# Optimization experiments

Hardware: AMD Instinct MI355X
Metric: run time of the kernel (lower is better)

The kernel has to match this reference:

```python
import jax, jax.numpy as jnp
import numpy as np

N_NODES = 100000
N_EDGES = 1600000
IN_DIM, HID_DIM, N_CLASSES = 128, 64, 40


def spmm(edge_row, edge_col, edge_val, dense):
    # sparse [N,N] @ dense [N,D] via gather + segment-sum over edges
    msgs = edge_val[:, None] * dense[edge_col]            # [E, D]
    return jax.ops.segment_sum(msgs, edge_row, num_segments=N_NODES)


def setup_inputs() -> dict:
    key = jax.random.key(0)
    ks = jax.random.split(key, 8)
    x = jax.random.normal(ks[0], (N_NODES, IN_DIM), dtype=jnp.float32)
    edge_row = jax.random.randint(ks[1], (N_EDGES,), 0, N_NODES, dtype=jnp.int32)
    edge_col = jax.random.randint(ks[2], (N_EDGES,), 0, N_NODES, dtype=jnp.int32)
    edge_val = jax.random.uniform(ks[3], (N_EDGES,), dtype=jnp.float32)
    s1 = 1.0 / np.sqrt(IN_DIM)
    s2 = 1.0 / np.sqrt(HID_DIM)
    W1 = jax.random.normal(ks[4], (IN_DIM, HID_DIM), dtype=jnp.float32) * s1
    b1 = jnp.zeros((HID_DIM,), dtype=jnp.float32)
    W2 = jax.random.normal(ks[5], (HID_DIM, HID_DIM), dtype=jnp.float32) * s2
    b2 = jnp.zeros((HID_DIM,), dtype=jnp.float32)
    Wc = jax.random.normal(ks[6], (HID_DIM, N_CLASSES), dtype=jnp.float32) * s2
    bc = jnp.zeros((N_CLASSES,), dtype=jnp.float32)
    return {"x": x, "edge_row": edge_row, "edge_col": edge_col, "edge_val": edge_val,
            "W1": W1, "b1": b1, "W2": W2, "b2": b2, "Wc": Wc, "bc": bc}


def reference(x, edge_row, edge_col, edge_val, W1, b1, W2, b2, Wc, bc):
    # GCN layer 1: support = xW+b, aggregate, relu  (dropout off in eval)
    h = jax.nn.relu(spmm(edge_row, edge_col, edge_val, x @ W1 + b1))
    # GCN layer 2
    h = spmm(edge_row, edge_col, edge_val, h @ W2 + b2)
    # node classifier + log-softmax
    logits = h @ Wc + bc
    return jax.nn.log_softmax(logits, axis=-1)
```

## Files before the change

kernel.cpp:

```cpp
#include <hip/hip_runtime.h>

#define N_NODES   100000
#define N_EDGES   1600000
#define IN_DIM    128
#define HID_DIM   64
#define N_CLASSES 40
#define U_DIM     40

#define NBUCK 782
#define BCAP  2816
#define EPB   6400
#define PBLK  1024
#define GRID_A 250

typedef __attribute__((ext_vector_type(8))) short bf16x8;
typedef __attribute__((ext_vector_type(4))) float f32x4;

__device__ inline short f2bf(float f) {
    unsigned u = __float_as_uint(f);
    unsigned r = (u + 0x7FFFu + ((u >> 16) & 1u)) >> 16;
    return (short)r;
}
__device__ inline float bflo(unsigned w) { return __uint_as_float(w << 16); }
__device__ inline float bfhi(unsigned w) { return __uint_as_float(w & 0xFFFF0000u); }
__device__ inline float upval(unsigned w) { return __uint_as_float((w >> 17) << 16); }

__global__ __launch_bounds__(PBLK) void prep_parta(const int* __restrict__ erow,
                                                   const int* __restrict__ ecol,
                                                   const float* __restrict__ eval,
                                                   int* __restrict__ bcnt,
                                                   int2* __restrict__ tmp,
                                                   const float* __restrict__ W1,
                                                   const float* __restrict__ W2,
                                                   const float* __restrict__ Wc,
                                                   const float* __restrict__ b2,
                                                   short* __restrict__ W1t,
                                                   short* __restrict__ Mt,
                                                   float* __restrict__ bv) {
    __shared__ int2 pay[EPB];
    __shared__ int hist[NBUCK], lbase[NBUCK], cur[NBUCK], dofs[NBUCK], scan[NBUCK];
    int tid = threadIdx.x;
    if (blockIdx.x >= GRID_A) {
        int pb = blockIdx.x - GRID_A;
        {
            int i = pb * PBLK + tid;
            if (i < IN_DIM * HID_DIM) {
                int n = i >> 7, k = i & 127;
                W1t[i] = f2bf(W1[k * HID_DIM + n]);
            }
        }
        if (pb == 0) {
            for (int idx = tid; idx < HID_DIM * HID_DIM; idx += PBLK) {
                int n = idx >> 6, i = idx & 63;
                float acc = 0.f;
                if (n < N_CLASSES)
                    for (int j = 0; j < HID_DIM; ++j)
                        acc = fmaf(W2[i * HID_DIM + j], Wc[j * N_CLASSES + n], acc);
                Mt[n * HID_DIM + i] = f2bf(acc);
            }
        }
        if (pb == 1 && tid < N_CLASSES) {
            float acc = 0.f;
            for (int j = 0; j < HID_DIM; ++j)
                acc = fmaf(b2[j], Wc[j * N_CLASSES + tid], acc);
            bv[tid] = acc;
        }
        return;
    }
    int e0 = blockIdx.x * EPB;
    for (int i = tid; i < NBUCK; i += PBLK) { hist[i] = 0; cur[i] = 0; }
    __syncthreads();
    for (int i = tid; i < EPB; i += PBLK)
        atomicAdd(&hist[erow[e0 + i] >> 7], 1);
    __syncthreads();
    for (int i = tid; i < NBUCK; i += PBLK) {
        int n = hist[i];
        dofs[i] = i * BCAP + (n ? atomicAdd(&bcnt[i], n) : 0);
        scan[i] = n;
    }
    __syncthreads();
    for (int off = 1; off < NBUCK; off <<= 1) {
        int t = 0;
        if (tid < NBUCK && tid >= off) t = scan[tid - off];
        __syncthreads();
        if (tid < NBUCK) scan[tid] += t;
        __syncthreads();
    }
    if (tid < NBUCK) {
        lbase[tid] = scan[tid] - hist[tid];
        dofs[tid] -= lbase[tid];
    }
    __syncthreads();
    for (int i = tid; i < EPB; i += PBLK) {
        int e = e0 + i;
        int r = erow[e];
        int b = r >> 7;
        int p = lbase[b] + atomicAdd(&cur[b], 1);
        unsigned u = __float_as_uint(eval[e]);
        unsigned vb = ((u + 0x7FFFu + ((u >> 16) & 1u)) >> 16) & 0x7FFFu;
        pay[p] = make_int2(((r & 127) << 17) | ecol[e], (int)((vb << 10) | (unsigned)b));
    }
    __syncthreads();
    for (int p = tid; p < EPB; p += PBLK) {
        int2 v = pay[p];
        int b = (unsigned)v.y & 1023u;
        int dest = dofs[b] + p;
        if (dest < (b + 1) * BCAP)
            tmp[dest] = v;
    }
}

__global__ __launch_bounds__(256) void part_b_gemm1(const int* __restrict__ bcnt,
                                                    const int2* __restrict__ tmp,
                                                    unsigned* __restrict__ tmp2,
                                                    int2* __restrict__ rowmeta,
                                                    const float* __restrict__ x,
                                                    const short* __restrict__ W1t,
                                                    const float* __restrict__ b1,
                                                    unsigned short* __restrict__ outH) {
    __shared__ int2 ein[BCAP];
    __shared__ unsigned eout[BCAP];
    __shared__ int hist[128], pad[128], basep[128], cur[128], scan[128];
    if (blockIdx.x < NBUCK) {
        int b = blockIdx.x;
        int nb = bcnt[b]; if (nb > BCAP) nb = BCAP;
        for (int i = threadIdx.x; i < nb; i += 256) ein[i] = tmp[(size_t)b * BCAP + i];
        if (threadIdx.x < 128) { hist[threadIdx.x] = 0; cur[threadIdx.x] = 0; }
        __syncthreads();
        for (int i = threadIdx.x; i < nb; i += 256)
            atomicAdd(&hist[(ein[i].x >> 17) & 127], 1);
        __syncthreads();
        if (threadIdx.x < 128) {
            pad[threadIdx.x] = (hist[threadIdx.x] + 3) & ~3;
            scan[threadIdx.x] = pad[threadIdx.x];
        }
        __syncthreads();
        for (int off = 1; off < 128; off <<= 1) {
            int t = 0;
            if (threadIdx.x < 128 && threadIdx.x >= off) t = scan[threadIdx.x - off];
            __syncthreads();
            if (threadIdx.x < 128) scan[threadIdx.x] += t;
            __syncthreads();
        }
        if (threadIdx.x < 128) basep[threadIdx.x] = scan[threadIdx.x] - pad[threadIdx.x];
        __syncthreads();
        int ntot = scan[127]; if (ntot > BCAP) ntot = BCAP;
        for (int i = threadIdx.x; i < nb; i += 256) {
            int lr = (ein[i].x >> 17) & 127;
            int p = basep[lr] + atomicAdd(&cur[lr], 1);
            if (p < BCAP) {
                unsigned vb = ((unsigned)ein[i].y >> 10) & 0x7FFFu;
                eout[p] = (vb << 17) | (unsigned)(ein[i].x & 0x1FFFF);
            }
        }
        __syncthreads();
        if (threadIdx.x < 128) {
            int pe = basep[threadIdx.x] + pad[threadIdx.x];
            for (int p = basep[threadIdx.x] + hist[threadIdx.x]; p < pe && p < BCAP; ++p)
                eout[p] = 0u;
        }
        __syncthreads();
        for (int i = threadIdx.x; i < ntot; i += 256) tmp2[(size_t)b * BCAP + i] = eout[i];
        if (threadIdx.x < 128) {
            int r = b * 128 + threadIdx.x;
            if (r < N_NODES)
                rowmeta[r] = make_int2(b * BCAP + basep[threadIdx.x], pad[threadIdx.x]);
        }
    } else {
        int gb = blockIdx.x - NBUCK;
        int wave = threadIdx.x >> 6;
        int lane = threadIdx.x & 63;
        int node0 = gb * 64 + wave * 16;
        if (node0 >= N_NODES) return;
        int m = lane & 15;
        int q = lane >> 4;
        const float* xrow = x + (size_t)(node0 + m) * IN_DIM;
        f32x4 acc0 = {0,0,0,0}, acc1 = {0,0,0,0}, acc2 = {0,0,0,0}, acc3 = {0,0,0,0};
#pragma unroll
        for (int kb = 0; kb < 4; ++kb) {
            int k0 = kb * 32 + q * 8;
            float4 a0 = *(const float4*)(xrow + k0);
            float4 a1 = *(const float4*)(xrow + k0 + 4);
            bf16x8 af;
            af[0]=f2bf(a0.x); af[1]=f2bf(a0.y); af[2]=f2bf(a0.z); af[3]=f2bf(a0.w);
            af[4]=f2bf(a1.x); af[5]=f2bf(a1.y); af[6]=f2bf(a1.z); af[7]=f2bf(a1.w);
            bf16x8 bf0 = *(const bf16x8*)(W1t + ( 0 + m) * IN_DIM + k0);
            bf16x8 bf1 = *(const bf16x8*)(W1t + (16 + m) * IN_DIM + k0);
            bf16x8 bf2 = *(const bf16x8*)(W1t + (32 + m) * IN_DIM + k0);
            bf16x8 bf3 = *(const bf16x8*)(W1t + (48 + m) * IN_DIM + k0);
            acc0 = __builtin_amdgcn_mfma_f32_16x16x32_bf16(af, bf0, acc0, 0, 0, 0);
            acc1 = __builtin_amdgcn_mfma_f32_16x16x32_bf16(af, bf1, acc1, 0, 0, 0);
            acc2 = __builtin_amdgcn_mfma_f32_16x16x32_bf16(af, bf2, acc2, 0, 0, 0);
            acc3 = __builtin_amdgcn_mfma_f32_16x16x32_bf16(af, bf3, acc3, 0, 0, 0);
        }
        f32x4 accs[4] = {acc0, acc1, acc2, acc3};
#pragma unroll
        for (int t = 0; t < 4; ++t) {
            float bias = b1[t * 16 + m];
#pragma unroll
            for (int r = 0; r < 4; ++r) {
                int node = node0 + q * 4 + r;
                outH[(size_t)node * HID_DIM + t * 16 + m] = (unsigned short)f2bf(accs[t][r] + bias);
            }
        }
    }
}

#define FMA8(v,g) \
    a0=fmaf(v,bflo(g.x),a0); a1=fmaf(v,bfhi(g.x),a1); a2=fmaf(v,bflo(g.y),a2); a3=fmaf(v,bfhi(g.y),a3); \
    a4=fmaf(v,bflo(g.z),a4); a5=fmaf(v,bfhi(g.z),a5); a6=fmaf(v,bflo(g.w),a6); a7=fmaf(v,bfhi(g.w),a7);

__global__ __launch_bounds__(256) void spmm1_mm(const int2* __restrict__ rowmeta,
                                                const unsigned* __restrict__ ecv,
                                                const unsigned short* __restrict__ dense,
                                                const short* __restrict__ Mt,
                                                unsigned short* __restrict__ outU) {
    __shared__ unsigned lm[4][8][68];
    __shared__ unsigned short tr[32][64];
    int wave = threadIdx.x >> 6;
    int lane = threadIdx.x & 63;
    int s = lane >> 3, dq = lane & 7;
    int row = wave * 8 + s;
    int r = blockIdx.x * 32 + row;
    int2 meta = rowmeta[r];
    int beg = meta.x, deg = meta.y;
    int degc = deg < 64 ? deg : 64;
    for (int e = dq * 2; e < degc; e += 16)
        *(uint2*)&lm[wave][s][e] = *(const uint2*)(ecv + beg + e);
    __syncthreads();
    const unsigned* mp = lm[wave][s];
    float a0=0,a1=0,a2=0,a3=0,a4=0,a5=0,a6=0,a7=0;
#define LDG(wv) (*(const uint4*)(dense + ((size_t)((wv) & 0x1FFFF) << 6) + (dq << 3)))
    if (deg > 0) {
        int e = 0;
        if (degc & 4) {
            uint4 w = *(const uint4*)mp;
            uint4 g0 = LDG(w.x), g1 = LDG(w.y), g2 = LDG(w.z), g3 = LDG(w.w);
            float v0 = upval(w.x), v1 = upval(w.y), v2 = upval(w.z), v3 = upval(w.w);
            FMA8(v0,g0); FMA8(v1,g1); FMA8(v2,g2); FMA8(v3,g3);
            e = 4;
        }
        for (; e < degc; e += 8) {
            uint4 wa = *(const uint4*)(mp + e);
            uint4 wb = *(const uint4*)(mp + e + 4);
            uint4 g0 = LDG(wa.x), g1 = LDG(wa.y), g2 = LDG(wa.z), g3 = LDG(wa.w);
            uint4 g4 = LDG(wb.x), g5 = LDG(wb.y), g6 = LDG(wb.z), g7 = LDG(wb.w);
            float v0 = upval(wa.x), v1 = upval(wa.y), v2 = upval(wa.z), v3 = upval(wa.w);
            float v4 = upval(wb.x), v5 = upval(wb.y), v6 = upval(wb.z), v7 = upval(wb.w);
            FMA8(v0,g0); FMA8(v1,g1); FMA8(v2,g2); FMA8(v3,g3);
            FMA8(v4,g4); FMA8(v5,g5); FMA8(v6,g6); FMA8(v7,g7);
        }
        for (int e2 = 64; e2 < deg; ++e2) {
            unsigned we = ecv[beg + e2];
            uint4 g = LDG(we);
            float v = upval(we);
            FMA8(v,g);
        }
    }
#undef LDG
    uint4 o;
    o.x = (unsigned short)f2bf(fmaxf(a0,0.f)) | ((unsigned)(unsigned short)f2bf(fmaxf(a1,0.f)) << 16);
    o.y = (unsigned short)f2bf(fmaxf(a2,0.f)) | ((unsigned)(unsigned short)f2bf(fmaxf(a3,0.f)) << 16);
    o.z = (unsigned short)f2bf(fmaxf(a4,0.f)) | ((unsigned)(unsigned short)f2bf(fmaxf(a5,0.f)) << 16);
    o.w = (unsigned short)f2bf(fmaxf(a6,0.f)) | ((unsigned)(unsigned short)f2bf(fmaxf(a7,0.f)) << 16);
    *(uint4*)(&tr[row][(dq ^ s) << 3]) = o;
    __syncthreads();
    int m = lane & 15;
    int q = lane >> 4;
    int nt = wave >> 1;
    int tb = (wave & 1) << 1;
    int arow = nt * 16 + m;
    f32x4 c0 = {0,0,0,0}, c1 = {0,0,0,0};
#pragma unroll
    for (int kb = 0; kb < 2; ++kb) {
        int ch = kb * 4 + q;
        bf16x8 af = *(const bf16x8*)(&tr[arow][(ch ^ (arow & 7)) << 3]);
        int k0 = kb * 32 + q * 8;
        bf16x8 bf0 = *(const bf16x8*)(Mt + ((tb + 0) * 16 + m) * HID_DIM + k0);
        bf16x8 bf1 = *(const bf16x8*)(Mt + ((tb + 1) * 16 + m) * HID_DIM + k0);
        c0 = __builtin_amdgcn_mfma_f32_16x16x32_bf16(af, bf0, c0, 0, 0, 0);
        c1 = __builtin_amdgcn_mfma_f32_16x16x32_bf16(af, bf1, c1, 0, 0, 0);
    }
#pragma unroll
    for (int rr = 0; rr < 4; ++rr) {
        int node = blockIdx.x * 32 + nt * 16 + q * 4 + rr;
        int col0 = tb * 16 + m;
        int col1 = col0 + 16;
        if (col0 < U_DIM)
            outU[(size_t)node * U_DIM + col0] = (unsigned short)f2bf(c0[rr]);
        if (col1 < U_DIM)
            outU[(size_t)node * U_DIM + col1] = (unsigned short)f2bf(c1[rr]);
    }
}

__global__ __launch_bounds__(256) void spmm_cls(const int2* __restrict__ rowmeta,
                                                const unsigned* __restrict__ ecv,
                                                const unsigned short* __restrict__ dense,
                                                const float* __restrict__ bv,
                                                const float* __restrict__ bc,
                                                float* __restrict__ outF) {
    __shared__ unsigned lm[4][8][68];
    int wave = threadIdx.x >> 6;
    int lane = threadIdx.x & 63;
    int s = lane >> 3, dq = lane & 7;
    int dof = (dq < 5 ? dq : 0) << 3;
    int r = (blockIdx.x * 4 + wave) * 8 + s;
    float4 bv0 = {0,0,0,0}, bv1 = {0,0,0,0}, bc0 = {0,0,0,0}, bc1 = {0,0,0,0};
    if (dq < 5) {
        bv0 = *(const float4*)(bv + dq * 8);  bv1 = *(const float4*)(bv + dq * 8 + 4);
        bc0 = *(const float4*)(bc + dq * 8);  bc1 = *(const float4*)(bc + dq * 8 + 4);
    }
    int2 meta = rowmeta[r];
    int beg = meta.x, deg = meta.y;
    int degc = deg < 64 ? deg : 64;
    for (int e = dq * 2; e < degc; e += 16)
        *(uint2*)&lm[wave][s][e] = *(const uint2*)(ecv + beg + e);
    __syncthreads();
    const unsigned* mp = lm[wave][s];
    float a0=0,a1=0,a2=0,a3=0,a4=0,a5=0,a6=0,a7=0, asum=0;
#define LDU(wv) (*(const uint4*)(dense + (size_t)((wv) & 0x1FFFF) * U_DIM + dof))
    if (deg > 0) {
        int e = 0;
        if (degc & 4) {
            uint4 w = *(const uint4*)mp;
            uint4 g0 = LDU(w.x), g1 = LDU(w.y), g2 = LDU(w.z), g3 = LDU(w.w);
            float v0 = upval(w.x), v1 = upval(w.y), v2 = upval(w.z), v3 = upval(w.w);
            asum += v0 + v1 + v2 + v3;
            FMA8(v0,g0); FMA8(v1,g1); FMA8(v2,g2); FMA8(v3,g3);
            e = 4;
        }
        for (; e < degc; e += 8) {
            uint4 wa = *(const uint4*)(mp + e);
            uint4 wb = *(const uint4*)(mp + e + 4);
            uint4 g0 = LDU(wa.x), g1 = LDU(wa.y), g2 = LDU(wa.z), g3 = LDU(wa.w);
            uint4 g4 = LDU(wb.x), g5 = LDU(wb.y), g6 = LDU(wb.z), g7 = LDU(wb.w);
            float v0 = upval(wa.x), v1 = upval(wa.y), v2 = upval(wa.z), v3 = upval(wa.w);
            float v4 = upval(wb.x), v5 = upval(wb.y), v6 = upval(wb.z), v7 = upval(wb.w);
            asum += v0 + v1 + v2 + v3 + v4 + v5 + v6 + v7;
            FMA8(v0,g0); FMA8(v1,g1); FMA8(v2,g2); FMA8(v3,g3);
            FMA8(v4,g4); FMA8(v5,g5); FMA8(v6,g6); FMA8(v7,g7);
        }
        for (int e2 = 64; e2 < deg; ++e2) {
            unsigned we = ecv[beg + e2];
            uint4 g = LDU(we);
            float v = upval(we);
            asum += v;
            FMA8(v,g);
        }
    }
#undef LDU
    float l0 = fmaf(asum, bv0.x, a0) + bc0.x;
    float l1 = fmaf(asum, bv0.y, a1) + bc0.y;
    float l2 = fmaf(asum, bv0.z, a2) + bc0.z;
    float l3 = fmaf(asum, bv0.w, a3) + bc0.w;
    float l4 = fmaf(asum, bv1.x, a4) + bc1.x;
    float l5 = fmaf(asum, bv1.y, a5) + bc1.y;
    float l6 = fmaf(asum, bv1.z, a6) + bc1.z;
    float l7 = fmaf(asum, bv1.w, a7) + bc1.w;
    float mx = -1e30f;
    if (dq < 5)
        mx = fmaxf(fmaxf(fmaxf(l0, l1), fmaxf(l2, l3)),
                   fmaxf(fmaxf(l4, l5), fmaxf(l6, l7)));
#pragma unroll
    for (int off = 1; off < 8; off <<= 1) mx = fmaxf(mx, __shfl_xor(mx, off));
    float ss = 0.f;
    if (dq < 5)
        ss = __expf(l0 - mx) + __expf(l1 - mx) + __expf(l2 - mx) + __expf(l3 - mx)
           + __expf(l4 - mx) + __expf(l5 - mx) + __expf(l6 - mx) + __expf(l7 - mx);
#pragma unroll
    for (int off = 1; off < 8; off <<= 1) ss += __shfl_xor(ss, off);
    float lse = mx + __logf(ss);
    if (dq < 5) {
        float4 o0 = {l0 - lse, l1 - lse, l2 - lse, l3 - lse};
        float4 o1 = {l4 - lse, l5 - lse, l6 - lse, l7 - lse};
        float* dst = outF + (size_t)r * N_CLASSES + dq * 8;
        *(float4*)(dst) = o0;
        *(float4*)(dst + 4) = o1;
    }
}

extern "C" void kernel_launch(void* const* d_in, const int* in_sizes, int n_in,
                              void* d_out, int out_size, void* d_ws, size_t ws_size,
                              hipStream_t stream) {
    const float* x    = (const float*)d_in[0];
    const int*   erow = (const int*)  d_in[1];
    const int*   ecol = (const int*)  d_in[2];
    const float* eval = (const float*)d_in[3];
    const float* W1   = (const float*)d_in[4];
    const float* b1   = (const float*)d_in[5];
    const float* W2   = (const float*)d_in[6];
    const float* b2   = (const float*)d_in[7];
    const float* Wc   = (const float*)d_in[8];
    const float* bc   = (const float*)d_in[9];
    float* out = (float*)d_out;

    char* ws = (char*)d_ws;
    size_t off = 0;
    auto alloc = [&](size_t bytes) { char* p = ws + off; off += (bytes + 255) & ~(size_t)255; return p; };
    unsigned short* bufA = (unsigned short*)alloc((size_t)N_NODES * HID_DIM * sizeof(short));
    unsigned short* bufB = (unsigned short*)alloc((size_t)N_NODES * U_DIM * sizeof(short));
    int2*     tmp     = (int2*)    alloc((size_t)NBUCK * BCAP * sizeof(int2));
    unsigned* tmp2    = (unsigned*)alloc((size_t)NBUCK * BCAP * sizeof(unsigned));
    int2*     rowmeta = (int2*)    alloc((size_t)N_NODES * sizeof(int2));
    int*      bcnt    = (int*)     alloc(NBUCK * sizeof(int));
    short*    W1t     = (short*)   alloc((size_t)IN_DIM * HID_DIM * sizeof(short));
    short*    Mt      = (short*)   alloc((size_t)HID_DIM * HID_DIM * sizeof(short));
    float*    bv      = (float*)   alloc(64 * sizeof(float));

    const int tile_grid = (N_NODES + 63) / 64;
    const int spmm_grid = N_NODES / 32;

    hipMemsetAsync(bcnt, 0, NBUCK * sizeof(int), stream);
    prep_parta<<<GRID_A + 8, PBLK, 0, stream>>>(erow, ecol, eval, bcnt, tmp,
                                                W1, W2, Wc, b2, W1t, Mt, bv);
    part_b_gemm1<<<NBUCK + tile_grid, 256, 0, stream>>>(bcnt, tmp, tmp2, rowmeta,
                                                        x, W1t, b1, bufA);
    spmm1_mm<<<spmm_grid, 256, 0, stream>>>(rowmeta, tmp2, bufA, Mt, bufB);
    spmm_cls<<<spmm_grid, 256, 0, stream>>>(rowmeta, tmp2, bufB, bv, bc, out);
}
```

Baseline: 218.4 us.

## Use wave-shuffle scans, halve edges per partition block, pad U rows to 64

```diff
diff --git a/kernel.cpp b/kernel.cpp
--- a/kernel.cpp
+++ b/kernel.cpp
@@ -6,12 +6,13 @@
 #define HID_DIM   64
 #define N_CLASSES 40
 #define U_DIM     40
+#define U_STRIDE  64
 
 #define NBUCK 782
 #define BCAP  2816
-#define EPB   6400
+#define EPB   3200
 #define PBLK  1024
-#define GRID_A 250
+#define GRID_A 500
 
 typedef __attribute__((ext_vector_type(8))) short bf16x8;
 typedef __attribute__((ext_vector_type(4))) float f32x4;
@@ -38,7 +39,8 @@
                                                    short* __restrict__ Mt,
                                                    float* __restrict__ bv) {
     __shared__ int2 pay[EPB];
-    __shared__ int hist[NBUCK], lbase[NBUCK], cur[NBUCK], dofs[NBUCK], scan[NBUCK];
+    __shared__ int hist[NBUCK], lbase[NBUCK], cur[NBUCK], dofs[NBUCK];
+    __shared__ int wscan[16];
     int tid = threadIdx.x;
     if (blockIdx.x >= GRID_A) {
         int pb = blockIdx.x - GRID_A;
@@ -76,19 +78,33 @@
     for (int i = tid; i < NBUCK; i += PBLK) {
         int n = hist[i];
         dofs[i] = i * BCAP + (n ? atomicAdd(&bcnt[i], n) : 0);
-        scan[i] = n;
-    }
-    __syncthreads();
-    for (int off = 1; off < NBUCK; off <<= 1) {
-        int t = 0;
-        if (tid < NBUCK && tid >= off) t = scan[tid - off];
-        __syncthreads();
-        if (tid < NBUCK) scan[tid] += t;
-        __syncthreads();
-    }
-    if (tid < NBUCK) {
-        lbase[tid] = scan[tid] - hist[tid];
-        dofs[tid] -= lbase[tid];
+    }
+    __syncthreads();
+    {
+        int lane = tid & 63, wv = tid >> 6;
+        int val = (tid < NBUCK) ? hist[tid] : 0;
+#pragma unroll
+        for (int off = 1; off < 64; off <<= 1) {
+            int t = __shfl_up(val, off);
+            if (lane >= off) val += t;
+        }
+        if (lane == 63) wscan[wv] = val;
+        __syncthreads();
+        if (wv == 0) {
+            int s = (lane < 16) ? wscan[lane] : 0;
+#pragma unroll
+            for (int off = 1; off < 16; off <<= 1) {
+                int t = __shfl_up(s, off);
+                if (lane >= off) s += t;
+            }
+            if (lane < 16) wscan[lane] = s;
+        }
+        __syncthreads();
+        if (tid < NBUCK) {
+            int incl = val + (wv ? wscan[wv - 1] : 0);
+            lbase[tid] = incl - hist[tid];
+            dofs[tid] -= lbase[tid];
+        }
     }
     __syncthreads();
     for (int i = tid; i < EPB; i += PBLK) {
@@ -120,7 +136,8 @@
                                                     unsigned short* __restrict__ outH) {
     __shared__ int2 ein[BCAP];
     __shared__ unsigned eout[BCAP];
-    __shared__ int hist[128], pad[128], basep[128], cur[128], scan[128];
+    __shared__ int hist[128], pad[128], basep[128], cur[128];
+    __shared__ int wsum2[2];
     if (blockIdx.x < NBUCK) {
         int b = blockIdx.x;
         int nb = bcnt[b]; if (nb > BCAP) nb = BCAP;
@@ -130,21 +147,27 @@
         for (int i = threadIdx.x; i < nb; i += 256)
             atomicAdd(&hist[(ein[i].x >> 17) & 127], 1);
         __syncthreads();
-        if (threadIdx.x < 128) {
+        if (threadIdx.x < 128)
             pad[threadIdx.x] = (hist[threadIdx.x] + 3) & ~3;
-            scan[threadIdx.x] = pad[threadIdx.x];
-        }
-        __syncthreads();
-        for (int off = 1; off < 128; off <<= 1) {
-            int t = 0;
-            if (threadIdx.x < 128 && threadIdx.x >= off) t = scan[threadIdx.x - off];
+        __syncthreads();
+        {
+            int lane = threadIdx.x & 63, wv2 = threadIdx.x >> 6;
+            int val = 0;
+            if (threadIdx.x < 128) {
+                val = pad[threadIdx.x];
+#pragma unroll
+                for (int off = 1; off < 64; off <<= 1) {
+                    int t = __shfl_up(val, off);
+                    if (lane >= off) val += t;
+                }
+                if (lane == 63) wsum2[wv2] = val;
+            }
             __syncthreads();
-            if (threadIdx.x < 128) scan[threadIdx.x] += t;
-            __syncthreads();
-        }
-        if (threadIdx.x < 128) basep[threadIdx.x] = scan[threadIdx.x] - pad[threadIdx.x];
-        __syncthreads();
-        int ntot = scan[127]; if (ntot > BCAP) ntot = BCAP;
+            if (threadIdx.x < 128)
+                basep[threadIdx.x] = val + (wv2 ? wsum2[0] : 0) - pad[threadIdx.x];
+        }
+        __syncthreads();
+        int ntot = wsum2[0] + wsum2[1]; if (ntot > BCAP) ntot = BCAP;
         for (int i = threadIdx.x; i < nb; i += 256) {
             int lr = (ein[i].x >> 17) & 127;
             int p = basep[lr] + atomicAdd(&cur[lr], 1);
@@ -287,9 +310,9 @@
         int col0 = tb * 16 + m;
         int col1 = col0 + 16;
         if (col0 < U_DIM)
-            outU[(size_t)node * U_DIM + col0] = (unsigned short)f2bf(c0[rr]);
+            outU[(size_t)node * U_STRIDE + col0] = (unsigned short)f2bf(c0[rr]);
         if (col1 < U_DIM)
-            outU[(size_t)node * U_DIM + col1] = (unsigned short)f2bf(c1[rr]);
+            outU[(size_t)node * U_STRIDE + col1] = (unsigned short)f2bf(c1[rr]);
     }
 }
 
@@ -318,7 +341,7 @@
     __syncthreads();
     const unsigned* mp = lm[wave][s];
     float a0=0,a1=0,a2=0,a3=0,a4=0,a5=0,a6=0,a7=0, asum=0;
-#define LDU(wv) (*(const uint4*)(dense + (size_t)((wv) & 0x1FFFF) * U_DIM + dof))
+#define LDU(wv) (*(const uint4*)(dense + ((size_t)((wv) & 0x1FFFF) << 6) + dof))
     if (deg > 0) {
         int e = 0;
         if (degc & 4) {
@@ -398,7 +421,7 @@
     size_t off = 0;
     auto alloc = [&](size_t bytes) { char* p = ws + off; off += (bytes + 255) & ~(size_t)255; return p; };
     unsigned short* bufA = (unsigned short*)alloc((size_t)N_NODES * HID_DIM * sizeof(short));
-    unsigned short* bufB = (unsigned short*)alloc((size_t)N_NODES * U_DIM * sizeof(short));
+    unsigned short* bufB = (unsigned short*)alloc((size_t)N_NODES * U_STRIDE * sizeof(short));
     int2*     tmp     = (int2*)    alloc((size_t)NBUCK * BCAP * sizeof(int2));
     unsigned* tmp2    = (unsigned*)alloc((size_t)NBUCK * BCAP * sizeof(unsigned));
     int2*     rowmeta = (int2*)    alloc((size_t)N_NODES * sizeof(int2));
```

Measured after the change: 225.6 us. 1.03x slower.
